# Kernel optimization log

Hardware: AMD Instinct MI355X
Metric: run time of the kernel (lower is better)

The kernel has to match this reference:

```python
import jax, jax.numpy as jnp
import numpy as np

B = 16384        # batch
P = 8            # num policies (experts)
D = 512          # latent dim
A = 64           # action dim
H = 1024         # hidden dim


def setup_inputs() -> dict:
    key = jax.random.key(0)
    ks = jax.random.split(key, 7)
    latents = jax.random.normal(ks[0], (B, D), dtype=jnp.float32)
    actions = jax.random.normal(ks[1], (B, A), dtype=jnp.float32)
    policy_indices = jax.random.randint(ks[2], (B,), 0, P, dtype=jnp.int64)
    # Per-policy 2-layer MLP params: concat(latent, action) -> hidden -> latent
    scale1 = 1.0 / np.sqrt(D + A)
    scale2 = 1.0 / np.sqrt(H)
    W1 = jax.random.normal(ks[3], (P, D + A, H), dtype=jnp.float32) * scale1
    b1 = jnp.zeros((P, H), dtype=jnp.float32)
    W2 = jax.random.normal(ks[4], (P, H, D), dtype=jnp.float32) * scale2
    b2 = jnp.zeros((P, D), dtype=jnp.float32)
    return {"latents": latents, "actions": actions, "policy_indices": policy_indices,
            "W1": W1, "b1": b1, "W2": W2, "b2": b2}


def reference(latents, actions, policy_indices, W1, b1, W2, b2):
    # Original: for each policy i, route rows with policy_indices == i through
    # that policy's dynamics model; scatter results back into next_latents.
    # Equivalent dense form: run all experts, then select per-row expert output.
    x = jnp.concatenate([latents, actions], axis=-1)          # [B, D+A]
    h = jax.nn.relu(jnp.einsum('bd,pdh->bph', x, W1) + b1)    # [B, P, H]
    y = jnp.einsum('bph,phd->bpd', h, W2) + b2                # [B, P, D]
    idx = policy_indices[:, None, None]                       # [B, 1, 1]
    next_latents = jnp.take_along_axis(y, idx, axis=1)[:, 0]  # [B, D]
    return next_latents
```

## Files before the change

### kernel.cpp

```cpp
#include <hip/hip_runtime.h>
#include <hip/hip_bf16.h>
#include <stdint.h>

#define B_SZ 16384
#define P_SZ 8
#define D_SZ 512
#define A_SZ 64
#define K1 576
#define H_SZ 1024
#define NSEG 64
#define MB_MAX 72
#define BPAD (B_SZ + P_SZ*256)
#define PREP_BLOCKS (BPAD * 72 / 256)
#define TRANS_BLOCKS (32 * 32 * 16)
#define G1_GRID (BPAD / 128 * (H_SZ / 128))
#define G2_GRID (BPAD / 128 * (D_SZ / 64))

typedef __bf16 bf16_t;
typedef __bf16 bf16x8 __attribute__((ext_vector_type(8)));
typedef float f32x4 __attribute__((ext_vector_type(4)));

__device__ __forceinline__ void glds16(const void* g, void* l) {
    __builtin_amdgcn_global_load_lds(
        (const __attribute__((address_space(1))) unsigned*)g,
        (__attribute__((address_space(3))) unsigned*)l, 16, 0, 0);
}


__global__ __launch_bounds__(256) void hist_block(const int* __restrict__ pol,
                                                  int* __restrict__ blockhist,
                                                  int* __restrict__ rowidx) {
    __shared__ int lc[P_SZ];
    int t = threadIdx.x;
    if (t < P_SZ) lc[t] = 0;
    __syncthreads();
    int gid = blockIdx.x * 256 + t;
    rowidx[gid] = -1;
    if (gid < BPAD - B_SZ) rowidx[B_SZ + gid] = -1;
    atomicAdd(&lc[pol[gid]], 1);
    __syncthreads();
    if (t < P_SZ) blockhist[blockIdx.x * P_SZ + t] = lc[t];
}

__global__ __launch_bounds__(64) void prefix_kernel(const int* __restrict__ blockhist,
                                                    int* __restrict__ counts,
                                                    int* __restrict__ cursors,
                                                    int* __restrict__ blk_p) {
    int t = threadIdx.x;
    if (t < P_SZ) {
        int s = 0;
        for (int b = 0; b < NSEG; ++b) s += blockhist[b * P_SZ + t];
        counts[t] = s;
    }
    __syncthreads();
    if (t == 0) {
        int run = 0;
        for (int p = 0; p < P_SZ; ++p) {
            cursors[p] = run;
            int nb = (counts[p] + 255) >> 8;
            for (int b = 0; b < nb; ++b) blk_p[(run >> 8) + b] = p;
            run += nb * 256;
        }
        for (int b = run >> 8; b < MB_MAX; ++b) blk_p[b] = -1;
    }
}

__global__ __launch_bounds__(256) void scatter_agg(const int* __restrict__ pol,
                                                   int* __restrict__ cursors,
                                                   int* __restrict__ rowidx) {
    __shared__ int lc[P_SZ], base_s[P_SZ];
    int t = threadIdx.x;
    if (t < P_SZ) lc[t] = 0;
    __syncthreads();
    int i = blockIdx.x * 256 + t;
    int p = pol[i];
    int lpos = atomicAdd(&lc[p], 1);
    __syncthreads();
    if (t < P_SZ) base_s[t] = atomicAdd(&cursors[t], lc[t]);
    __syncthreads();
    rowidx[base_s[p] + lpos] = i;
}


__global__ __launch_bounds__(256) void prep_all(const float* __restrict__ latents,
                                                const float* __restrict__ actions,
                                                const int* __restrict__ rowidx,
                                                const float* __restrict__ W1,
                                                const float* __restrict__ W2,
                                                bf16_t* __restrict__ xs,
                                                bf16_t* __restrict__ w1t,
                                                bf16_t* __restrict__ w2t) {
    int bx = blockIdx.x;
    int tid = threadIdx.x;
    if (bx < PREP_BLOCKS) {
        int idx = bx * 256 + tid;
        int s = idx / 72;
        int col = (idx - s * 72) * 8;
        int g = rowidx[s];
        bf16x8 o;
        if (g < 0) {
            o = (bf16x8){0,0,0,0,0,0,0,0};
        } else {
            const float* src;
            if (col < D_SZ) src = latents + (size_t)g * D_SZ + col;
            else            src = actions + (size_t)g * A_SZ + (col - D_SZ);
            f32x4 v0 = *(const f32x4*)src;
            f32x4 v1 = *(const f32x4*)(src + 4);
            o[0] = (bf16_t)v0[0]; o[1] = (bf16_t)v0[1]; o[2] = (bf16_t)v0[2]; o[3] = (bf16_t)v0[3];
            o[4] = (bf16_t)v1[0]; o[5] = (bf16_t)v1[1]; o[6] = (bf16_t)v1[2]; o[7] = (bf16_t)v1[3];
        }
        *(bf16x8*)(xs + (size_t)s * K1 + col) = o;
        return;
    }
    int tz = bx - PREP_BLOCKS;
    int z = tz >> 10;
    int rem = tz & 1023;
    int k0 = (rem & 31) * 32, n0 = (rem >> 5) * 32;
    int K = (z < P_SZ) ? K1 : H_SZ;
    int N = (z < P_SZ) ? H_SZ : D_SZ;
    if (k0 >= K || n0 >= N) return;
    int p = z & 7;
    const float* Wp = ((z < P_SZ) ? W1 : W2) + (size_t)p * K * N;
    bf16_t* WTp = ((z < P_SZ) ? w1t : w2t) + (size_t)p * N * K;
    __shared__ float ls[32][33];
    {
        int kk = tid >> 3, nn = (tid & 7) * 4;
        f32x4 v = *(const f32x4*)&Wp[(size_t)(k0 + kk) * N + n0 + nn];
        ls[kk][nn]     = v[0];
        ls[kk][nn + 1] = v[1];
        ls[kk][nn + 2] = v[2];
        ls[kk][nn + 3] = v[3];
    }
    __syncthreads();
#pragma unroll
    for (int e = 0; e < 2; ++e) {
        int idx = e * 256 + tid;
        int nn = idx >> 4, kp = (idx & 15) * 2;
        union { bf16_t h[2]; unsigned u; } pk;
        pk.h[0] = (bf16_t)ls[kp][nn];
        pk.h[1] = (bf16_t)ls[kp + 1][nn];
        *(unsigned*)&WTp[(size_t)(n0 + nn) * K + k0 + kp] = pk.u;
    }
}


__global__ __launch_bounds__(256, 3) void gemm1_kernel(
    const bf16_t* __restrict__ xs, const bf16_t* __restrict__ w1t,
    const float* __restrict__ b1, const int* __restrict__ blk_p,
    bf16_t* __restrict__ h) {

    const int b = blockIdx.x;
    const int wid = (b & 7) * (G1_GRID / 8) + (b >> 3);
    const int mb = wid >> 3;
    const int nb = wid & 7;
    const int p = blk_p[mb >> 1];
    if (p < 0) return;
    const int m0 = mb * 128;
    const int n0 = nb * 128;

    __shared__ __align__(16) bf16_t As[128 * 32];
    __shared__ __align__(16) bf16_t Bs[128 * 32];

    const int tid = threadIdx.x;
    const int wave = tid >> 6, lane = tid & 63;

    const bf16_t* a_src[2]; bf16_t* a_dst[2];
#pragma unroll
    for (int i = 0; i < 2; ++i) {
        int c = (wave * 2 + i) * 64 + lane;
        int r = c >> 2;
        int kl = (c & 3) ^ ((r >> 1) & 3);
        a_src[i] = xs + (size_t)(m0 + r) * K1 + kl * 8;
        a_dst[i] = As + c * 8;
    }
    const bf16_t* b_src[2]; bf16_t* b_dst[2];
#pragma unroll
    for (int i = 0; i < 2; ++i) {
        int c = (wave * 2 + i) * 64 + lane;
        int r = c >> 2;
        int kl = (c & 3) ^ ((r >> 1) & 3);
        b_src[i] = w1t + ((size_t)p * H_SZ + n0 + r) * K1 + kl * 8;
        b_dst[i] = Bs + c * 8;
    }

    const int l16 = lane & 15, qd = lane >> 4;
    const int swz = (l16 >> 1) & 3;
    const int wr = wave >> 1, wc = wave & 1;
    int aoff[4], boff[4];
#pragma unroll
    for (int i = 0; i < 4; ++i) aoff[i] = (wr * 64 + i * 16 + l16) * 32 + ((qd ^ swz) * 8);
#pragma unroll
    for (int j = 0; j < 4; ++j) boff[j] = (wc * 64 + j * 16 + l16) * 32 + ((qd ^ swz) * 8);

    f32x4 acc[4][4];
#pragma unroll
    for (int i = 0; i < 4; ++i)
#pragma unroll
        for (int j = 0; j < 4; ++j)
            acc[i][j] = (f32x4){0.f, 0.f, 0.f, 0.f};

    for (int kt = 0; kt < K1; kt += 32) {
        __syncthreads();
#pragma unroll
        for (int i = 0; i < 2; ++i) glds16(a_src[i] + kt, a_dst[i]);
#pragma unroll
        for (int i = 0; i < 2; ++i) glds16(b_src[i] + kt, b_dst[i]);
        __syncthreads();
        bf16x8 af[4], bfv[4];
#pragma unroll
        for (int i = 0; i < 4; ++i) af[i] = *(const bf16x8*)(As + aoff[i]);
#pragma unroll
        for (int j = 0; j < 4; ++j) bfv[j] = *(const bf16x8*)(Bs + boff[j]);
#pragma unroll
        for (int i = 0; i < 4; ++i)
#pragma unroll
            for (int j = 0; j < 4; ++j)
                acc[i][j] = __builtin_amdgcn_mfma_f32_16x16x32_bf16(af[i], bfv[j], acc[i][j], 0, 0, 0);
    }

#pragma unroll
    for (int i = 0; i < 4; ++i) {
#pragma unroll
        for (int r = 0; r < 4; ++r) {
            int ml = wr * 64 + i * 16 + qd * 4 + r;
            size_t row = (size_t)(m0 + ml);
#pragma unroll
            for (int j = 0; j < 4; ++j) {
                int n = n0 + wc * 64 + j * 16 + l16;
                float v = acc[i][j][r] + b1[p * H_SZ + n];
                h[row * H_SZ + n] = (bf16_t)fmaxf(v, 0.f);
            }
        }
    }
}

__global__ __launch_bounds__(256, 4) void gemm2_kernel(
    const bf16_t* __restrict__ h, const bf16_t* __restrict__ w2t,
    const float* __restrict__ b2, const int* __restrict__ blk_p,
    const int* __restrict__ rowidx, float* __restrict__ out) {

    const int b = blockIdx.x;
    const int wid = (b & 7) * (G2_GRID / 8) + (b >> 3);
    const int mb = wid >> 3;
    const int nb = wid & 7;
    const int p = blk_p[mb >> 1];
    if (p < 0) return;
    const int m0 = mb * 128;
    const int n0 = nb * 64;

    __shared__ __align__(16) bf16_t As[128 * 32];
    __shared__ __align__(16) bf16_t Bs[64 * 32];

    const int tid = threadIdx.x;
    const int wave = tid >> 6, lane = tid & 63;

    const bf16_t* a_src[2]; bf16_t* a_dst[2];
#pragma unroll
    for (int i = 0; i < 2; ++i) {
        int c = (wave * 2 + i) * 64 + lane;
        int r = c >> 2;
        int kl = (c & 3) ^ ((r >> 1) & 3);
        a_src[i] = h + (size_t)(m0 + r) * H_SZ + kl * 8;
        a_dst[i] = As + c * 8;
    }
    const bf16_t* b_src0; bf16_t* b_dst0;
    {
        int c = wave * 64 + lane;
        int r = c >> 2;
        int kl = (c & 3) ^ ((r >> 1) & 3);
        b_src0 = w2t + ((size_t)p * D_SZ + n0 + r) * H_SZ + kl * 8;
        b_dst0 = Bs + c * 8;
    }

    const int l16 = lane & 15, qd = lane >> 4;
    const int swz = (l16 >> 1) & 3;
    const int wr = wave >> 1, wc = wave & 1;
    int aoff[4], boff[2];
#pragma unroll
    for (int i = 0; i < 4; ++i) aoff[i] = (wr * 64 + i * 16 + l16) * 32 + ((qd ^ swz) * 8);
#pragma unroll
    for (int j = 0; j < 2; ++j) boff[j] = (wc * 32 + j * 16 + l16) * 32 + ((qd ^ swz) * 8);

    f32x4 acc[4][2];
#pragma unroll
    for (int i = 0; i < 4; ++i)
#pragma unroll
        for (int j = 0; j < 2; ++j)
            acc[i][j] = (f32x4){0.f, 0.f, 0.f, 0.f};

    for (int kt = 0; kt < H_SZ; kt += 32) {
        __syncthreads();
#pragma unroll
        for (int i = 0; i < 2; ++i) glds16(a_src[i] + kt, a_dst[i]);
        glds16(b_src0 + kt, b_dst0);
        __syncthreads();
        bf16x8 af[4], bfv[2];
#pragma unroll
        for (int i = 0; i < 4; ++i) af[i] = *(const bf16x8*)(As + aoff[i]);
#pragma unroll
        for (int j = 0; j < 2; ++j) bfv[j] = *(const bf16x8*)(Bs + boff[j]);
#pragma unroll
        for (int i = 0; i < 4; ++i)
#pragma unroll
            for (int j = 0; j < 2; ++j)
                acc[i][j] = __builtin_amdgcn_mfma_f32_16x16x32_bf16(af[i], bfv[j], acc[i][j], 0, 0, 0);
    }

#pragma unroll
    for (int i = 0; i < 4; ++i) {
#pragma unroll
        for (int r = 0; r < 4; ++r) {
            int ml = wr * 64 + i * 16 + qd * 4 + r;
            int g = rowidx[m0 + ml];
            if (g >= 0) {
                size_t orow = (size_t)g * D_SZ;
#pragma unroll
                for (int j = 0; j < 2; ++j) {
                    int n = n0 + wc * 32 + j * 16 + l16;
                    out[orow + n] = acc[i][j][r] + b2[p * D_SZ + n];
                }
            }
        }
    }
}


extern "C" void kernel_launch(void* const* d_in, const int* in_sizes, int n_in,
                              void* d_out, int out_size, void* d_ws, size_t ws_size,
                              hipStream_t stream) {
    const float* latents = (const float*)d_in[0];
    const float* actions = (const float*)d_in[1];
    const int*   pol     = (const int*)d_in[2];
    const float* W1      = (const float*)d_in[3];
    const float* b1      = (const float*)d_in[4];
    const float* W2      = (const float*)d_in[5];
    const float* b2      = (const float*)d_in[6];
    float* out = (float*)d_out;

    char* ws = (char*)d_ws;
    int* counts    = (int*)ws;
    int* cursors   = counts + P_SZ;
    int* blk_p     = cursors + P_SZ;
    int* blockhist = blk_p + MB_MAX;
    int* rowidx    = blockhist + NSEG * P_SZ;
    size_t pos = ((size_t)(2 * P_SZ + MB_MAX + NSEG * P_SZ + BPAD) * sizeof(int) + 255) & ~(size_t)255;
    bf16_t* xs  = (bf16_t*)(ws + pos);  pos += (size_t)BPAD * K1 * 2;
    bf16_t* hbuf= (bf16_t*)(ws + pos);  pos += (size_t)BPAD * H_SZ * 2;
    bf16_t* w1t = (bf16_t*)(ws + pos);  pos += (size_t)P_SZ * H_SZ * K1 * 2;
    bf16_t* w2t = (bf16_t*)(ws + pos);  pos += (size_t)P_SZ * D_SZ * H_SZ * 2;

    hist_block<<<NSEG, 256, 0, stream>>>(pol, blockhist, rowidx);
    prefix_kernel<<<1, 64, 0, stream>>>(blockhist, counts, cursors, blk_p);
    scatter_agg<<<NSEG, 256, 0, stream>>>(pol, cursors, rowidx);
    prep_all<<<PREP_BLOCKS + TRANS_BLOCKS, 256, 0, stream>>>(
        latents, actions, rowidx, W1, W2, xs, w1t, w2t);
    gemm1_kernel<<<G1_GRID, 256, 0, stream>>>(xs, w1t, b1, blk_p, hbuf);
    gemm2_kernel<<<G2_GRID, 256, 0, stream>>>(hbuf, w2t, b2, blk_p, rowidx, out);
}
```

Measured before the change: 201.1 us.

## Double GEMM K-tile depth, enlarge weight transpose tiles, parallelize prefix scan

Both grouped GEMMs now stage 64-wide K slices per barrier pair, as two 32-wide swizzled sub-tiles, which halves the number of block synchronizations per tile. The weight transpose uses 64x64 tiles with 16-byte bf16 stores and no idle blocks. The prefix kernel replaces serial per-policy loops with a shuffle reduction and a parallel fill of the block-to-policy map. The larger LDS footprint (32KB in gemm1) may reduce occupancy below the launch-bounds target of 3 blocks.

```diff
diff --git a/kernel.cpp b/kernel.cpp
--- a/kernel.cpp
+++ b/kernel.cpp
@@ -12,7 +12,8 @@
 #define MB_MAX 72
 #define BPAD (B_SZ + P_SZ*256)
 #define PREP_BLOCKS (BPAD * 72 / 256)
-#define TRANS_BLOCKS (32 * 32 * 16)
+#define TR1_BLOCKS (P_SZ * 9 * 16)
+#define TR2_BLOCKS (P_SZ * 16 * 8)
 #define G1_GRID (BPAD / 128 * (H_SZ / 128))
 #define G2_GRID (BPAD / 128 * (D_SZ / 64))
 
@@ -42,26 +43,35 @@
     if (t < P_SZ) blockhist[blockIdx.x * P_SZ + t] = lc[t];
 }
 
-__global__ __launch_bounds__(64) void prefix_kernel(const int* __restrict__ blockhist,
-                                                    int* __restrict__ counts,
-                                                    int* __restrict__ cursors,
-                                                    int* __restrict__ blk_p) {
+__global__ __launch_bounds__(256) void prefix_kernel(const int* __restrict__ blockhist,
+                                                     int* __restrict__ counts,
+                                                     int* __restrict__ cursors,
+                                                     int* __restrict__ blk_p) {
+    __shared__ int csh[P_SZ];
     int t = threadIdx.x;
-    if (t < P_SZ) {
-        int s = 0;
-        for (int b = 0; b < NSEG; ++b) s += blockhist[b * P_SZ + t];
-        counts[t] = s;
-    }
+    int p = t >> 5, i = t & 31;
+    int s = blockhist[i * P_SZ + p] + blockhist[(i + 32) * P_SZ + p];
+#pragma unroll
+    for (int m = 16; m >= 1; m >>= 1) s += __shfl_xor(s, m, 32);
+    if (i == 0) csh[p] = s;
     __syncthreads();
     if (t == 0) {
         int run = 0;
-        for (int p = 0; p < P_SZ; ++p) {
-            cursors[p] = run;
-            int nb = (counts[p] + 255) >> 8;
-            for (int b = 0; b < nb; ++b) blk_p[(run >> 8) + b] = p;
-            run += nb * 256;
-        }
-        for (int b = run >> 8; b < MB_MAX; ++b) blk_p[b] = -1;
+        for (int pp = 0; pp < P_SZ; ++pp) {
+            counts[pp] = csh[pp];
+            cursors[pp] = run;
+            run += ((csh[pp] + 255) >> 8) * 256;
+        }
+    }
+    if (t < MB_MAX) {
+        int run = 0, val = -1;
+#pragma unroll
+        for (int pp = 0; pp < P_SZ; ++pp) {
+            int nb = (csh[pp] + 255) >> 8;
+            if (t >= run && t < run + nb) val = pp;
+            run += nb;
+        }
+        blk_p[t] = val;
     }
 }
 
@@ -113,18 +123,26 @@
         return;
     }
     int tz = bx - PREP_BLOCKS;
-    int z = tz >> 10;
-    int rem = tz & 1023;
-    int k0 = (rem & 31) * 32, n0 = (rem >> 5) * 32;
-    int K = (z < P_SZ) ? K1 : H_SZ;
-    int N = (z < P_SZ) ? H_SZ : D_SZ;
-    if (k0 >= K || n0 >= N) return;
-    int p = z & 7;
-    const float* Wp = ((z < P_SZ) ? W1 : W2) + (size_t)p * K * N;
-    bf16_t* WTp = ((z < P_SZ) ? w1t : w2t) + (size_t)p * N * K;
-    __shared__ float ls[32][33];
-    {
-        int kk = tid >> 3, nn = (tid & 7) * 4;
+    const float* Wp; bf16_t* WTp; int K, N, k0, n0;
+    if (tz < TR1_BLOCKS) {
+        int p = tz / 144, rem = tz % 144;
+        k0 = (rem / 16) * 64; n0 = (rem % 16) * 64;
+        K = K1; N = H_SZ;
+        Wp = W1 + (size_t)p * K1 * H_SZ;
+        WTp = w1t + (size_t)p * H_SZ * K1;
+    } else {
+        int u = tz - TR1_BLOCKS;
+        int p = u / 128, rem = u % 128;
+        k0 = (rem / 8) * 64; n0 = (rem % 8) * 64;
+        K = H_SZ; N = D_SZ;
+        Wp = W2 + (size_t)p * H_SZ * D_SZ;
+        WTp = w2t + (size_t)p * D_SZ * H_SZ;
+    }
+    __shared__ float ls[64][65];
+#pragma unroll
+    for (int e = 0; e < 4; ++e) {
+        int idx = e * 256 + tid;
+        int kk = idx >> 4, nn = (idx & 15) * 4;
         f32x4 v = *(const f32x4*)&Wp[(size_t)(k0 + kk) * N + n0 + nn];
         ls[kk][nn]     = v[0];
         ls[kk][nn + 1] = v[1];
@@ -135,11 +153,11 @@
 #pragma unroll
     for (int e = 0; e < 2; ++e) {
         int idx = e * 256 + tid;
-        int nn = idx >> 4, kp = (idx & 15) * 2;
-        union { bf16_t h[2]; unsigned u; } pk;
-        pk.h[0] = (bf16_t)ls[kp][nn];
-        pk.h[1] = (bf16_t)ls[kp + 1][nn];
-        *(unsigned*)&WTp[(size_t)(n0 + nn) * K + k0 + kp] = pk.u;
+        int nn = idx >> 3, ks = (idx & 7) * 8;
+        bf16x8 o;
+#pragma unroll
+        for (int q = 0; q < 8; ++q) o[q] = (bf16_t)ls[ks + q][nn];
+        *(bf16x8*)&WTp[(size_t)(n0 + nn) * K + k0 + ks] = o;
     }
 }
 
@@ -158,30 +176,27 @@
     const int m0 = mb * 128;
     const int n0 = nb * 128;
 
-    __shared__ __align__(16) bf16_t As[128 * 32];
-    __shared__ __align__(16) bf16_t Bs[128 * 32];
+    constexpr int SUB = 128 * 32;
+    __shared__ __align__(16) bf16_t As[2 * SUB];
+    __shared__ __align__(16) bf16_t Bs[2 * SUB];
 
     const int tid = threadIdx.x;
     const int wave = tid >> 6, lane = tid & 63;
 
-    const bf16_t* a_src[2]; bf16_t* a_dst[2];
-#pragma unroll
-    for (int i = 0; i < 2; ++i) {
-        int c = (wave * 2 + i) * 64 + lane;
-        int r = c >> 2;
-        int kl = (c & 3) ^ ((r >> 1) & 3);
-        a_src[i] = xs + (size_t)(m0 + r) * K1 + kl * 8;
-        a_dst[i] = As + c * 8;
-    }
-    const bf16_t* b_src[2]; bf16_t* b_dst[2];
-#pragma unroll
-    for (int i = 0; i < 2; ++i) {
-        int c = (wave * 2 + i) * 64 + lane;
-        int r = c >> 2;
-        int kl = (c & 3) ^ ((r >> 1) & 3);
-        b_src[i] = w1t + ((size_t)p * H_SZ + n0 + r) * K1 + kl * 8;
-        b_dst[i] = Bs + c * 8;
-    }
+    const bf16_t *a_src[2][2], *b_src[2][2];
+    bf16_t *a_dst[2][2], *b_dst[2][2];
+#pragma unroll
+    for (int hh = 0; hh < 2; ++hh)
+#pragma unroll
+        for (int i = 0; i < 2; ++i) {
+            int c = (wave * 2 + i) * 64 + lane;
+            int r = c >> 2;
+            int kl = (c & 3) ^ ((r >> 1) & 3);
+            a_src[hh][i] = xs + (size_t)(m0 + r) * K1 + hh * 32 + kl * 8;
+            a_dst[hh][i] = As + hh * SUB + c * 8;
+            b_src[hh][i] = w1t + ((size_t)p * H_SZ + n0 + r) * K1 + hh * 32 + kl * 8;
+            b_dst[hh][i] = Bs + hh * SUB + c * 8;
+        }
 
     const int l16 = lane & 15, qd = lane >> 4;
     const int swz = (l16 >> 1) & 3;
@@ -199,23 +214,29 @@
         for (int j = 0; j < 4; ++j)
             acc[i][j] = (f32x4){0.f, 0.f, 0.f, 0.f};
 
-    for (int kt = 0; kt < K1; kt += 32) {
+    for (int kt = 0; kt < K1; kt += 64) {
         __syncthreads();
 #pragma unroll
-        for (int i = 0; i < 2; ++i) glds16(a_src[i] + kt, a_dst[i]);
-#pragma unroll
-        for (int i = 0; i < 2; ++i) glds16(b_src[i] + kt, b_dst[i]);
+        for (int hh = 0; hh < 2; ++hh)
+#pragma unroll
+            for (int i = 0; i < 2; ++i) {
+                glds16(a_src[hh][i] + kt, a_dst[hh][i]);
+                glds16(b_src[hh][i] + kt, b_dst[hh][i]);
+            }
         __syncthreads();
-        bf16x8 af[4], bfv[4];
-#pragma unroll
-        for (int i = 0; i < 4; ++i) af[i] = *(const bf16x8*)(As + aoff[i]);
-#pragma unroll
-        for (int j = 0; j < 4; ++j) bfv[j] = *(const bf16x8*)(Bs + boff[j]);
-#pragma unroll
-        for (int i = 0; i < 4; ++i)
-#pragma unroll
-            for (int j = 0; j < 4; ++j)
-                acc[i][j] = __builtin_amdgcn_mfma_f32_16x16x32_bf16(af[i], bfv[j], acc[i][j], 0, 0, 0);
+#pragma unroll
+        for (int hh = 0; hh < 2; ++hh) {
+            bf16x8 af[4], bfv[4];
+#pragma unroll
+            for (int i = 0; i < 4; ++i) af[i] = *(const bf16x8*)(As + hh * SUB + aoff[i]);
+#pragma unroll
+            for (int j = 0; j < 4; ++j) bfv[j] = *(const bf16x8*)(Bs + hh * SUB + boff[j]);
+#pragma unroll
+            for (int i = 0; i < 4; ++i)
+#pragma unroll
+                for (int j = 0; j < 4; ++j)
+                    acc[i][j] = __builtin_amdgcn_mfma_f32_16x16x32_bf16(af[i], bfv[j], acc[i][j], 0, 0, 0);
+        }
     }
 
 #pragma unroll
@@ -248,28 +269,33 @@
     const int m0 = mb * 128;
     const int n0 = nb * 64;
 
-    __shared__ __align__(16) bf16_t As[128 * 32];
-    __shared__ __align__(16) bf16_t Bs[64 * 32];
+    constexpr int ASUB = 128 * 32;
+    constexpr int BSUB = 64 * 32;
+    __shared__ __align__(16) bf16_t As[2 * ASUB];
+    __shared__ __align__(16) bf16_t Bs[2 * BSUB];
 
     const int tid = threadIdx.x;
     const int wave = tid >> 6, lane = tid & 63;
 
-    const bf16_t* a_src[2]; bf16_t* a_dst[2];
-#pragma unroll
-    for (int i = 0; i < 2; ++i) {
-        int c = (wave * 2 + i) * 64 + lane;
-        int r = c >> 2;
-        int kl = (c & 3) ^ ((r >> 1) & 3);
-        a_src[i] = h + (size_t)(m0 + r) * H_SZ + kl * 8;
-        a_dst[i] = As + c * 8;
-    }
-    const bf16_t* b_src0; bf16_t* b_dst0;
-    {
+    const bf16_t *a_src[2][2]; bf16_t *a_dst[2][2];
+#pragma unroll
+    for (int hh = 0; hh < 2; ++hh)
+#pragma unroll
+        for (int i = 0; i < 2; ++i) {
+            int c = (wave * 2 + i) * 64 + lane;
+            int r = c >> 2;
+            int kl = (c & 3) ^ ((r >> 1) & 3);
+            a_src[hh][i] = h + (size_t)(m0 + r) * H_SZ + hh * 32 + kl * 8;
+            a_dst[hh][i] = As + hh * ASUB + c * 8;
+        }
+    const bf16_t *b_src[2]; bf16_t *b_dst[2];
+#pragma unroll
+    for (int hh = 0; hh < 2; ++hh) {
         int c = wave * 64 + lane;
         int r = c >> 2;
         int kl = (c & 3) ^ ((r >> 1) & 3);
-        b_src0 = w2t + ((size_t)p * D_SZ + n0 + r) * H_SZ + kl * 8;
-        b_dst0 = Bs + c * 8;
+        b_src[hh] = w2t + ((size_t)p * D_SZ + n0 + r) * H_SZ + hh * 32 + kl * 8;
+        b_dst[hh] = Bs + hh * BSUB + c * 8;
     }
 
     const int l16 = lane & 15, qd = lane >> 4;
@@ -288,22 +314,28 @@
         for (int j = 0; j < 2; ++j)
             acc[i][j] = (f32x4){0.f, 0.f, 0.f, 0.f};
 
-    for (int kt = 0; kt < H_SZ; kt += 32) {
+    for (int kt = 0; kt < H_SZ; kt += 64) {
         __syncthreads();
 #pragma unroll
-        for (int i = 0; i < 2; ++i) glds16(a_src[i] + kt, a_dst[i]);
-        glds16(b_src0 + kt, b_dst0);
+        for (int hh = 0; hh < 2; ++hh) {
+#pragma unroll
+            for (int i = 0; i < 2; ++i) glds16(a_src[hh][i] + kt, a_dst[hh][i]);
+            glds16(b_src[hh] + kt, b_dst[hh]);
+        }
         __syncthreads();
-        bf16x8 af[4], bfv[2];
-#pragma unroll
-        for (int i = 0; i < 4; ++i) af[i] = *(const bf16x8*)(As + aoff[i]);
-#pragma unroll
-        for (int j = 0; j < 2; ++j) bfv[j] = *(const bf16x8*)(Bs + boff[j]);
-#pragma unroll
-        for (int i = 0; i < 4; ++i)
-#pragma unroll
-            for (int j = 0; j < 2; ++j)
-                acc[i][j] = __builtin_amdgcn_mfma_f32_16x16x32_bf16(af[i], bfv[j], acc[i][j], 0, 0, 0);
+#pragma unroll
+        for (int hh = 0; hh < 2; ++hh) {
+            bf16x8 af[4], bfv[2];
+#pragma unroll
+            for (int i = 0; i < 4; ++i) af[i] = *(const bf16x8*)(As + hh * ASUB + aoff[i]);
+#pragma unroll
+            for (int j = 0; j < 2; ++j) bfv[j] = *(const bf16x8*)(Bs + hh * BSUB + boff[j]);
+#pragma unroll
+            for (int i = 0; i < 4; ++i)
+#pragma unroll
+                for (int j = 0; j < 2; ++j)
+                    acc[i][j] = __builtin_amdgcn_mfma_f32_16x16x32_bf16(af[i], bfv[j], acc[i][j], 0, 0, 0);
+        }
     }
 
 #pragma unroll
@@ -350,9 +382,9 @@
     bf16_t* w2t = (bf16_t*)(ws + pos);  pos += (size_t)P_SZ * D_SZ * H_SZ * 2;
 
     hist_block<<<NSEG, 256, 0, stream>>>(pol, blockhist, rowidx);
-    prefix_kernel<<<1, 64, 0, stream>>>(blockhist, counts, cursors, blk_p);
+    prefix_kernel<<<1, 256, 0, stream>>>(blockhist, counts, cursors, blk_p);
     scatter_agg<<<NSEG, 256, 0, stream>>>(pol, cursors, rowidx);
-    prep_all<<<PREP_BLOCKS + TRANS_BLOCKS, 256, 0, stream>>>(
+    prep_all<<<PREP_BLOCKS + TR1_BLOCKS + TR2_BLOCKS, 256, 0, stream>>>(
         latents, actions, rowidx, W1, W2, xs, w1t, w2t);
     gemm1_kernel<<<G1_GRID, 256, 0, stream>>>(xs, w1t, b1, blk_p, hbuf);
     gemm2_kernel<<<G2_GRID, 256, 0, stream>>>(hbuf, w2t, b2, blk_p, rowidx, out);
```

After: 192.6 us, median of 2. 1.04x faster.
